# Optimization experiments

Measured on AMD Instinct MI355X. Metric: run time of the kernel, lower is better.

## Reference

```python
import jax, jax.numpy as jnp
import numpy as np

C_S, C_Z, N_HEADS = 768, 64, 12
HEAD_DIM = C_S // N_HEADS
L = 1024
EPS = 1e-5


def _ln(x, g, b):
    mu = jnp.mean(x, axis=-1, keepdims=True)
    var = jnp.mean((x - mu) ** 2, axis=-1, keepdims=True)
    return (x - mu) * jax.lax.rsqrt(var + EPS) * g + b


def setup_inputs() -> dict:
    key = jax.random.key(0)
    ks = jax.random.split(key, 12)
    w = lambda k, shp, fan_in: jax.random.normal(k, shp, dtype=jnp.float32) / np.sqrt(fan_in)
    return {
        "single": jax.random.normal(ks[0], (L, C_S), dtype=jnp.float32),
        "pair": jax.random.normal(ks[1], (L, L, C_Z), dtype=jnp.float32),
        "ln_s_g": jnp.ones((C_S,), jnp.float32),
        "ln_s_b": jnp.zeros((C_S,), jnp.float32),
        "ln_z_g": jnp.ones((C_Z,), jnp.float32),
        "ln_z_b": jnp.zeros((C_Z,), jnp.float32),
        "Wq": w(ks[2], (C_S, C_S), C_S),
        "Wk": w(ks[3], (C_S, C_S), C_S),
        "Wv": w(ks[4], (C_S, C_S), C_S),
        "Wb": w(ks[5], (C_Z, N_HEADS), C_Z),
        "Wout": w(ks[6], (C_S, C_S), C_S),
        "bout": jnp.zeros((C_S,), jnp.float32),
        "Wgate": w(ks[7], (C_S, C_S), C_S),
        "bgate": jnp.zeros((C_S,), jnp.float32),
    }


def reference(single, pair, ln_s_g, ln_s_b, ln_z_g, ln_z_b,
              Wq, Wk, Wv, Wb, Wout, bout, Wgate, bgate):
    Lq = single.shape[0]
    s = _ln(single, ln_s_g, ln_s_b)                    # [L, C_S]
    z = _ln(pair, ln_z_g, ln_z_b)                      # [L, L, C_Z]
    q = (s @ Wq).reshape(Lq, N_HEADS, HEAD_DIM)
    k = (s @ Wk).reshape(Lq, N_HEADS, HEAD_DIM)
    v = (s @ Wv).reshape(Lq, N_HEADS, HEAD_DIM)
    logits = jnp.einsum('ihd,jhd->hij', q, k) / np.sqrt(HEAD_DIM)
    logits = logits + jnp.einsum('ijc,ch->hij', z, Wb)  # pair bias per head
    attn = jax.nn.softmax(logits, axis=-1)              # [H, L, L]
    out = jnp.einsum('hij,jhd->ihd', attn, v).reshape(Lq, C_S)
    return single + jax.nn.sigmoid(s @ Wgate + bgate) * (out @ Wout + bout)
```

## Files before the change

### kernel.cpp

```cpp
#include <hip/hip_runtime.h>

#define LQ 1024
#define CS 768
#define CZ 64
#define NH 12
#define HD 64

typedef float4 f4;
using bf16x8 = __attribute__((ext_vector_type(8))) short;
using f32x4  = __attribute__((ext_vector_type(4))) float;

static __device__ __forceinline__ unsigned short f2bf(float f) {
  unsigned int u = __float_as_uint(f);
  u += 0x7fffu + ((u >> 16) & 1u);
  return (unsigned short)(u >> 16);
}
static __device__ __forceinline__ float bf2f(unsigned short b) {
  return __uint_as_float(((unsigned int)b) << 16);
}
static __device__ __forceinline__ unsigned cvtpk(float lo, float hi) {
  unsigned r;
  asm("v_cvt_pk_bf16_f32 %0, %1, %2" : "=v"(r) : "v"(lo), "v"(hi));
  return r;
}

__global__ __launch_bounds__(256) void ln_wconv_k(
    const float* __restrict__ x, const float* __restrict__ g,
    const float* __restrict__ b, unsigned short* __restrict__ s_out,
    const float* __restrict__ Wq, const float* __restrict__ Wk,
    const float* __restrict__ Wv, const float* __restrict__ Wg,
    const float* __restrict__ Wo, unsigned short* __restrict__ wt) {
  const int bid = blockIdx.x;
  const int t = threadIdx.x;
  if (bid < LQ) {
    const int row = bid;
    const float* xr = x + (size_t)row * CS;
    float v0 = xr[t], v1 = xr[t + 256], v2 = xr[t + 512];
    float s1 = v0 + v1 + v2;
    float s2 = v0 * v0 + v1 * v1 + v2 * v2;
#pragma unroll
    for (int m = 1; m < 64; m <<= 1) {
      s1 += __shfl_xor(s1, m);
      s2 += __shfl_xor(s2, m);
    }
    __shared__ float r1[4], r2[4];
    const int wid = t >> 6;
    if ((t & 63) == 0) { r1[wid] = s1; r2[wid] = s2; }
    __syncthreads();
    s1 = r1[0] + r1[1] + r1[2] + r1[3];
    s2 = r2[0] + r2[1] + r2[2] + r2[3];
    const float mu = s1 * (1.f / CS);
    const float var = s2 * (1.f / CS) - mu * mu;
    const float rs = rsqrtf(var + 1e-5f);
    s_out[(size_t)row * CS + t]       = f2bf((v0 - mu) * rs * g[t]       + b[t]);
    s_out[(size_t)row * CS + t + 256] = f2bf((v1 - mu) * rs * g[t + 256] + b[t + 256]);
    s_out[(size_t)row * CS + t + 512] = f2bf((v2 - mu) * rs * g[t + 512] + b[t + 512]);
  } else {
    int r = bid - LQ;
    const int bz = r / 144; r %= 144;
    const int n0 = (r % 12) * 64, k0 = (r / 12) * 64;
    const float* W;
    switch (bz) {
      case 0: W = Wq; break;
      case 1: W = Wk; break;
      case 2: W = Wv; break;
      case 3: W = Wg; break;
      default: W = Wo; break;
    }
    unsigned short* o = wt + (size_t)bz * CS * CS;
    __shared__ float T[64][68];
    {
      const int rr = t >> 4, c = (t & 15) * 4;
#pragma unroll
      for (int u = 0; u < 4; ++u) {
        const f4 v = *(const f4*)&W[(size_t)(k0 + rr + u * 16) * CS + n0 + c];
        *(f4*)&T[rr + u * 16][c] = v;
      }
    }
    __syncthreads();
    {
      const int rn = t >> 2, ck = (t & 3) * 16;
      __align__(16) unsigned short tmp[16];
#pragma unroll
      for (int u = 0; u < 16; ++u) tmp[u] = f2bf(T[ck + u][rn]);
      unsigned short* dst = &o[(size_t)(n0 + rn) * CS + k0 + ck];
      *(uint4*)dst = ((const uint4*)tmp)[0];
      *(uint4*)(dst + 8) = ((const uint4*)tmp)[1];
    }
  }
}

__global__ __launch_bounds__(256) void pair_k(
    const float* __restrict__ pair, const float* __restrict__ zg,
    const float* __restrict__ zb, const float* __restrict__ Wb,
    unsigned short* __restrict__ biasF) {
  const int bid = blockIdx.x;
  const int t = threadIdx.x;
  const int w = t >> 6, lane = t & 63, g = lane >> 4, c = lane & 15;
  const int i0 = (bid >> 3) * 4;
  const int j0 = (bid & 7) * 128;
  const int il = c & 3, jl = c >> 2;
  const int irow = i0 + il;
  const int g2 = g * 2;
  const int gi = i0 >> 4, ga = (i0 >> 2) & 3;
  const size_t hd_base = ((size_t)gi * 16) * 4 * 256 + (size_t)ga * 64;

  const int csafe = (c < NH) ? c : 0;
  float C1 = 0.f, C2 = 0.f;
  for (int ch = 0; ch < CZ; ++ch) {
    const float wv = (c < NH) ? Wb[ch * NH + csafe] : 0.f;
    C1 = fmaf(zg[ch], wv, C1);
    C2 = fmaf(zb[ch], wv, C2);
  }
  bf16x8 wf0, wf1;
#pragma unroll
  for (int u = 0; u < 8; ++u) {
    const float w0 = (c < NH) ? zg[g * 8 + u] * Wb[(g * 8 + u) * NH + csafe] : 0.f;
    const float w1 = (c < NH) ? zg[32 + g * 8 + u] * Wb[(32 + g * 8 + u) * NH + csafe] : 0.f;
    wf0[u] = (short)f2bf(w0);
    wf1[u] = (short)f2bf(w1);
  }

  f32x4 p00, p01, p02, p03;
  f32x4 p10, p11, p12, p13;
  {
    const f32x4* s0 = (const f32x4*)(pair + ((size_t)irow * LQ + (j0 + w * 32 + jl)) * CZ);
    p00 = s0[g2]; p01 = s0[g2 + 1]; p02 = s0[g2 + 8]; p03 = s0[g2 + 9];
  }
#pragma unroll
  for (int it = 0; it < 8; ++it) {
    const bool useA = (it & 1) == 0;
    if (it < 7) {
      const f32x4* sn = (const f32x4*)(pair + ((size_t)irow * LQ + (j0 + w * 32 + (it + 1) * 4 + jl)) * CZ);
      if (useA) { p10 = sn[g2]; p11 = sn[g2 + 1]; p12 = sn[g2 + 8]; p13 = sn[g2 + 9]; }
      else      { p00 = sn[g2]; p01 = sn[g2 + 1]; p02 = sn[g2 + 8]; p03 = sn[g2 + 9]; }
    }
    const f32x4 x0a = useA ? p00 : p10;
    const f32x4 x0b = useA ? p01 : p11;
    const f32x4 x1a = useA ? p02 : p12;
    const f32x4 x1b = useA ? p03 : p13;

    float s1 = (((x0a[0] + x0a[1]) + (x0a[2] + x0a[3])) + ((x0b[0] + x0b[1]) + (x0b[2] + x0b[3])))
             + (((x1a[0] + x1a[1]) + (x1a[2] + x1a[3])) + ((x1b[0] + x1b[1]) + (x1b[2] + x1b[3])));
    float s2 = (((x0a[0]*x0a[0] + x0a[1]*x0a[1]) + (x0a[2]*x0a[2] + x0a[3]*x0a[3]))
             +  ((x0b[0]*x0b[0] + x0b[1]*x0b[1]) + (x0b[2]*x0b[2] + x0b[3]*x0b[3])))
             + (((x1a[0]*x1a[0] + x1a[1]*x1a[1]) + (x1a[2]*x1a[2] + x1a[3]*x1a[3]))
             +  ((x1b[0]*x1b[0] + x1b[1]*x1b[1]) + (x1b[2]*x1b[2] + x1b[3]*x1b[3])));
    s1 += __shfl_xor(s1, 16); s1 += __shfl_xor(s1, 32);
    s2 += __shfl_xor(s2, 16); s2 += __shfl_xor(s2, 32);
    const float mu = s1 * (1.f / CZ);
    const float var = s2 * (1.f / CZ) - mu * mu;
    const float rs = rsqrtf(var + 1e-5f);
    const float mup = -rs * mu;

    union { unsigned u[4]; bf16x8 v8; } A, B;
    A.u[0] = cvtpk(x0a[0], x0a[1]); A.u[1] = cvtpk(x0a[2], x0a[3]);
    A.u[2] = cvtpk(x0b[0], x0b[1]); A.u[3] = cvtpk(x0b[2], x0b[3]);
    B.u[0] = cvtpk(x1a[0], x1a[1]); B.u[1] = cvtpk(x1a[2], x1a[3]);
    B.u[2] = cvtpk(x1b[0], x1b[1]); B.u[3] = cvtpk(x1b[2], x1b[3]);

    f32x4 dd = (f32x4){0.f, 0.f, 0.f, 0.f};
    dd = __builtin_amdgcn_mfma_f32_16x16x32_bf16(A.v8, wf0, dd, 0, 0, 0);
    dd = __builtin_amdgcn_mfma_f32_16x16x32_bf16(B.v8, wf1, dd, 0, 0, 0);

    const float rr0 = __shfl(rs, g * 4 + 0), mm0 = __shfl(mup, g * 4 + 0);
    const float rr1 = __shfl(rs, g * 4 + 1), mm1 = __shfl(mup, g * 4 + 1);
    const float rr2 = __shfl(rs, g * 4 + 2), mm2 = __shfl(mup, g * 4 + 2);
    const float rr3 = __shfl(rs, g * 4 + 3), mm3 = __shfl(mup, g * 4 + 3);

    if (c < NH) {
      const float b0 = fmaf(rr0, dd[0], fmaf(mm0, C1, C2));
      const float b1 = fmaf(rr1, dd[1], fmaf(mm1, C1, C2));
      const float b2 = fmaf(rr2, dd[2], fmaf(mm2, C1, C2));
      const float b3 = fmaf(rr3, dd[3], fmaf(mm3, C1, C2));
      const int jj = j0 + w * 32 + it * 4 + g;
      const size_t base = ((size_t)c * 64) * 16384
                        + hd_base
                        + (size_t)(jj >> 6) * 1024
                        + (size_t)((jj >> 4) & 3) * 256
                        + (jj & 15) * 4;
      uint2 st;
      st.x = cvtpk(b0, b1);
      st.y = cvtpk(b2, b3);
      *(uint2*)&biasF[base] = st;
    }
  }
}

__global__ __launch_bounds__(256) void gemm_qkvg_k(
    const unsigned short* __restrict__ s, const unsigned short* __restrict__ wt,
    const float* __restrict__ bg,
    unsigned short* __restrict__ qb, unsigned short* __restrict__ kb,
    unsigned short* __restrict__ vt, float* __restrict__ gpre) {
  __shared__ __align__(16) unsigned short As[64][88];
  __shared__ __align__(16) unsigned short Bs[128][88];
  const int t = threadIdx.x;
  const int w = t >> 6, lane = t & 63, g = lane >> 4, c = lane & 15;
  const int wm = w >> 1, wn = w & 1;
  const int bx = blockIdx.x % 24, by = blockIdx.x / 24;
  const int m0 = by * 64;
  const int wid = bx / 6;
  const int nl0 = (bx % 6) * 128;
  const unsigned short* B = wt + (size_t)wid * CS * CS;

  f32x4 acc[2][4];
#pragma unroll
  for (int i = 0; i < 2; ++i)
#pragma unroll
    for (int j = 0; j < 4; ++j) acc[i][j] = (f32x4){0.f, 0.f, 0.f, 0.f};

  const int sra = t >> 2, sha = (t & 3) * 16;
  const int srb = t >> 1, shb = (t & 1) * 32;
  for (int kt = 0; kt < CS; kt += 64) {
    __syncthreads();
#pragma unroll
    for (int u = 0; u < 2; ++u)
      *(uint4*)&As[sra][sha + u * 8] = *(const uint4*)&s[(size_t)(m0 + sra) * CS + kt + sha + u * 8];
#pragma unroll
    for (int u = 0; u < 4; ++u)
      *(uint4*)&Bs[srb][shb + u * 8] = *(const uint4*)&B[(size_t)(nl0 + srb) * CS + kt + shb + u * 8];
    __syncthreads();
#pragma unroll
    for (int kk = 0; kk < 64; kk += 32) {
      bf16x8 af[2], bfr[4];
#pragma unroll
      for (int i = 0; i < 2; ++i) af[i] = *(const bf16x8*)&As[wm * 32 + i * 16 + c][kk + g * 8];
#pragma unroll
      for (int j = 0; j < 4; ++j) bfr[j] = *(const bf16x8*)&Bs[wn * 64 + j * 16 + c][kk + g * 8];
#pragma unroll
      for (int i = 0; i < 2; ++i)
#pragma unroll
        for (int j = 0; j < 4; ++j)
          acc[i][j] = __builtin_amdgcn_mfma_f32_16x16x32_bf16(af[i], bfr[j], acc[i][j], 0, 0, 0);
    }
  }
#pragma unroll
  for (int i = 0; i < 2; ++i) {
#pragma unroll
    for (int j = 0; j < 4; ++j) {
      const int mb = m0 + wm * 32 + i * 16 + g * 4;
      const int nn = nl0 + wn * 64 + j * 16 + c;
      const f32x4 a = acc[i][j];
      if (wid == 0) {
#pragma unroll
        for (int r = 0; r < 4; ++r) qb[(size_t)(mb + r) * CS + nn] = f2bf(a[r] * 0.125f);
      } else if (wid == 1) {
#pragma unroll
        for (int r = 0; r < 4; ++r) kb[(size_t)(mb + r) * CS + nn] = f2bf(a[r]);
      } else if (wid == 2) {
        ushort4 pk;
        pk.x = f2bf(a[0]); pk.y = f2bf(a[1]); pk.z = f2bf(a[2]); pk.w = f2bf(a[3]);
        *(ushort4*)&vt[(size_t)nn * LQ + mb] = pk;
      } else {
        const float bb = bg[nn];
#pragma unroll
        for (int r = 0; r < 4; ++r) gpre[(size_t)(mb + r) * CS + nn] = a[r] + bb;
      }
    }
  }
}

__global__ __launch_bounds__(256) void attn_k(
    const unsigned short* __restrict__ q, const unsigned short* __restrict__ k,
    const unsigned short* __restrict__ vt, const unsigned short* __restrict__ biasF,
    float* __restrict__ Opart, float* __restrict__ ml) {
  __shared__ __align__(16) unsigned short Qs[64][88];
  __shared__ __align__(16) unsigned short Ks[2][64][88];
  __shared__ __align__(16) unsigned short Vts[2][64][88];
  __shared__ __align__(16) unsigned short Ps[4][16][88];
  const int bx = blockIdx.x, h = blockIdx.y, z = blockIdx.z;
  const int i0 = bx * 64;
  const int jb = z * 512;
  const int t = threadIdx.x;
  const int w = t >> 6, lane = t & 63, g = lane >> 4, c = lane & 15;
  const int sr = t >> 2, sc = (t & 3) * 16;

#pragma unroll
  for (int u = 0; u < 2; ++u) {
    *(uint4*)&Qs[sr][sc + u * 8]     = *(const uint4*)&q[(size_t)(i0 + sr) * CS + h * HD + sc + u * 8];
    *(uint4*)&Ks[0][sr][sc + u * 8]  = *(const uint4*)&k[(size_t)(jb + sr) * CS + h * HD + sc + u * 8];
    *(uint4*)&Vts[0][sr][sc + u * 8] = *(const uint4*)&vt[(size_t)(h * HD + sr) * LQ + jb + sc + u * 8];
  }
  const size_t bbase = ((((size_t)h * 64 + (bx * 4 + w)) * 16 + (size_t)z * 8) * 4) * 256 + lane * 4;
  ushort4 bcur[4];
#pragma unroll
  for (int nb = 0; nb < 4; ++nb) bcur[nb] = *(const ushort4*)&biasF[bbase + nb * 256];
  __syncthreads();

  const bf16x8 aq0 = *(const bf16x8*)&Qs[w * 16 + c][g * 8];
  const bf16x8 aq1 = *(const bf16x8*)&Qs[w * 16 + c][32 + g * 8];

  f32x4 acc_o[4];
#pragma unroll
  for (int nb = 0; nb < 4; ++nb) acc_o[nb] = (f32x4){0.f, 0.f, 0.f, 0.f};
  float m_run[4] = {-1e30f, -1e30f, -1e30f, -1e30f};
  float l_run[4] = {0.f, 0.f, 0.f, 0.f};

  for (int jt = 0; jt < 8; ++jt) {
    const int cur = jt & 1;
    uint4 kr0, kr1, vr0, vr1;
    ushort4 bnx[4];
    if (jt < 7) {
      const int jn = jb + (jt + 1) * 64;
      kr0 = *(const uint4*)&k[(size_t)(jn + sr) * CS + h * HD + sc];
      kr1 = *(const uint4*)&k[(size_t)(jn + sr) * CS + h * HD + sc + 8];
      vr0 = *(const uint4*)&vt[(size_t)(h * HD + sr) * LQ + jn + sc];
      vr1 = *(const uint4*)&vt[(size_t)(h * HD + sr) * LQ + jn + sc + 8];
#pragma unroll
      for (int nb = 0; nb < 4; ++nb)
        bnx[nb] = *(const ushort4*)&biasF[bbase + (size_t)(jt + 1) * 1024 + nb * 256];
    }

    f32x4 sa[4];
#pragma unroll
    for (int nb = 0; nb < 4; ++nb) {
      f32x4 ci;
      ci[0] = bf2f(bcur[nb].x); ci[1] = bf2f(bcur[nb].y);
      ci[2] = bf2f(bcur[nb].z); ci[3] = bf2f(bcur[nb].w);
      const bf16x8 b0 = *(const bf16x8*)&Ks[cur][nb * 16 + c][g * 8];
      const bf16x8 b1 = *(const bf16x8*)&Ks[cur][nb * 16 + c][32 + g * 8];
      ci = __builtin_amdgcn_mfma_f32_16x16x32_bf16(aq0, b0, ci, 0, 0, 0);
      ci = __builtin_amdgcn_mfma_f32_16x16x32_bf16(aq1, b1, ci, 0, 0, 0);
      sa[nb] = ci;
    }

    float mt[4];
#pragma unroll
    for (int r = 0; r < 4; ++r) {
      float v = fmaxf(fmaxf(sa[0][r], sa[1][r]), fmaxf(sa[2][r], sa[3][r]));
      v = fmaxf(v, __shfl_xor(v, 1));
      v = fmaxf(v, __shfl_xor(v, 2));
      v = fmaxf(v, __shfl_xor(v, 4));
      v = fmaxf(v, __shfl_xor(v, 8));
      mt[r] = v;
    }
    float scale[4], ps[4];
#pragma unroll
    for (int r = 0; r < 4; ++r) {
      const float mn = fmaxf(m_run[r], mt[r]);
      scale[r] = __expf(m_run[r] - mn);
      m_run[r] = mn;
      ps[r] = 0.f;
    }
#pragma unroll
    for (int nb = 0; nb < 4; ++nb) {
#pragma unroll
      for (int r = 0; r < 4; ++r) {
        const float p = __expf(sa[nb][r] - m_run[r]);
        ps[r] += p;
        Ps[w][g * 4 + r][nb * 16 + c] = f2bf(p);
      }
    }
#pragma unroll
    for (int r = 0; r < 4; ++r) {
      float v = ps[r];
      v += __shfl_xor(v, 1);
      v += __shfl_xor(v, 2);
      v += __shfl_xor(v, 4);
      v += __shfl_xor(v, 8);
      l_run[r] = l_run[r] * scale[r] + v;
#pragma unroll
      for (int nb = 0; nb < 4; ++nb) acc_o[nb][r] *= scale[r];
    }

#pragma unroll
    for (int kb = 0; kb < 2; ++kb) {
      const bf16x8 pa = *(const bf16x8*)&Ps[w][c][kb * 32 + g * 8];
#pragma unroll
      for (int nb = 0; nb < 4; ++nb) {
        const bf16x8 bv = *(const bf16x8*)&Vts[cur][nb * 16 + c][kb * 32 + g * 8];
        acc_o[nb] = __builtin_amdgcn_mfma_f32_16x16x32_bf16(pa, bv, acc_o[nb], 0, 0, 0);
      }
    }

    if (jt < 7) {
      *(uint4*)&Ks[cur ^ 1][sr][sc]      = kr0;
      *(uint4*)&Ks[cur ^ 1][sr][sc + 8]  = kr1;
      *(uint4*)&Vts[cur ^ 1][sr][sc]     = vr0;
      *(uint4*)&Vts[cur ^ 1][sr][sc + 8] = vr1;
      __syncthreads();
#pragma unroll
      for (int nb = 0; nb < 4; ++nb) bcur[nb] = bnx[nb];
    }
  }

  const size_t rowb = (size_t)(z * NH + h) * LQ + i0 + w * 16 + g * 4;
#pragma unroll
  for (int nb = 0; nb < 4; ++nb)
#pragma unroll
    for (int r = 0; r < 4; ++r)
      Opart[(rowb + r) * HD + nb * 16 + c] = acc_o[nb][r];
  if (c == 0) {
#pragma unroll
    for (int r = 0; r < 4; ++r) {
      ml[(rowb + r) * 2]     = m_run[r];
      ml[(rowb + r) * 2 + 1] = l_run[r];
    }
  }
}

__global__ __launch_bounds__(256) void combine_k(
    const float* __restrict__ Opart, const float* __restrict__ ml,
    unsigned short* __restrict__ attno) {
  const int t = threadIdx.x;
  const int row = blockIdx.x * 4 + (t >> 6);
  const int d = t & 63;
  const int h = row >> 10, i = row & 1023;
  const size_t r0 = (size_t)h * LQ + i;
  const size_t r1 = (size_t)(NH + h) * LQ + i;
  const float m0 = ml[r0 * 2], l0 = ml[r0 * 2 + 1];
  const float m1 = ml[r1 * 2], l1 = ml[r1 * 2 + 1];
  const float M = fmaxf(m0, m1);
  const float a0 = __expf(m0 - M), a1 = __expf(m1 - M);
  const float L = a0 * l0 + a1 * l1;
  const float o = (a0 * Opart[r0 * HD + d] + a1 * Opart[r1 * HD + d]) / L;
  attno[(size_t)i * CS + h * HD + d] = f2bf(o);
}

__global__ __launch_bounds__(256) void gemm_final_k(
    const unsigned short* __restrict__ A, const unsigned short* __restrict__ wt,
    const float* __restrict__ bout, const float* __restrict__ single,
    const float* __restrict__ gpre, float* __restrict__ out) {
  __shared__ __align__(16) unsigned short As[64][88];
  __shared__ __align__(16) unsigned short Bs[128][88];
  const int t = threadIdx.x;
  const int wave = t >> 6, lane = t & 63, g = lane >> 4, c = lane & 15;
  const int wm = wave >> 1, wn = wave & 1;
  const int m0 = blockIdx.y * 64;
  const int nl0 = blockIdx.x * 128;
  const unsigned short* B = wt + (size_t)4 * CS * CS;

  f32x4 acc[2][4];
#pragma unroll
  for (int i = 0; i < 2; ++i)
#pragma unroll
    for (int j = 0; j < 4; ++j) acc[i][j] = (f32x4){0.f, 0.f, 0.f, 0.f};

  const int sra = t >> 2, sha = (t & 3) * 16;
  const int srb = t >> 1, shb = (t & 1) * 32;
  for (int kt = 0; kt < CS; kt += 64) {
    __syncthreads();
#pragma unroll
    for (int u = 0; u < 2; ++u)
      *(uint4*)&As[sra][sha + u * 8] = *(const uint4*)&A[(size_t)(m0 + sra) * CS + kt + sha + u * 8];
#pragma unroll
    for (int u = 0; u < 4; ++u)
      *(uint4*)&Bs[srb][shb + u * 8] = *(const uint4*)&B[(size_t)(nl0 + srb) * CS + kt + shb + u * 8];
    __syncthreads();
#pragma unroll
    for (int kk = 0; kk < 64; kk += 32) {
      bf16x8 af[2], bfr[4];
#pragma unroll
      for (int i = 0; i < 2; ++i) af[i] = *(const bf16x8*)&As[wm * 32 + i * 16 + c][kk + g * 8];
#pragma unroll
      for (int j = 0; j < 4; ++j) bfr[j] = *(const bf16x8*)&Bs[wn * 64 + j * 16 + c][kk + g * 8];
#pragma unroll
      for (int i = 0; i < 2; ++i)
#pragma unroll
        for (int j = 0; j < 4; ++j)
          acc[i][j] = __builtin_amdgcn_mfma_f32_16x16x32_bf16(af[i], bfr[j], acc[i][j], 0, 0, 0);
    }
  }

#pragma unroll
  for (int i = 0; i < 2; ++i) {
#pragma unroll
    for (int j = 0; j < 4; ++j) {
      const int mb = m0 + wm * 32 + i * 16 + g * 4;
      const int nn = nl0 + wn * 64 + j * 16 + c;
      const float bb = bout[nn];
      const f32x4 a = acc[i][j];
#pragma unroll
      for (int r = 0; r < 4; ++r) {
        const size_t idx = (size_t)(mb + r) * CS + nn;
        const float gate = 1.f / (1.f + __expf(-gpre[idx]));
        out[idx] = single[idx] + gate * (a[r] + bb);
      }
    }
  }
}

extern "C" void kernel_launch(void* const* d_in, const int* in_sizes, int n_in,
                              void* d_out, int out_size, void* d_ws, size_t ws_size,
                              hipStream_t stream) {
  const float* single = (const float*)d_in[0];
  const float* pair   = (const float*)d_in[1];
  const float* ln_s_g = (const float*)d_in[2];
  const float* ln_s_b = (const float*)d_in[3];
  const float* ln_z_g = (const float*)d_in[4];
  const float* ln_z_b = (const float*)d_in[5];
  const float* Wq     = (const float*)d_in[6];
  const float* Wk     = (const float*)d_in[7];
  const float* Wv     = (const float*)d_in[8];
  const float* Wb     = (const float*)d_in[9];
  const float* Wout   = (const float*)d_in[10];
  const float* bout   = (const float*)d_in[11];
  const float* Wgate  = (const float*)d_in[12];
  const float* bgate  = (const float*)d_in[13];
  float* out = (float*)d_out;

  unsigned short* s_bf  = (unsigned short*)d_ws;
  unsigned short* wt    = s_bf  + (size_t)LQ * CS;
  unsigned short* q_bf  = wt    + (size_t)5 * CS * CS;
  unsigned short* k_bf  = q_bf  + (size_t)LQ * CS;
  unsigned short* vt_bf = k_bf  + (size_t)LQ * CS;
  unsigned short* attno = vt_bf + (size_t)CS * LQ;
  unsigned short* biasF = attno + (size_t)LQ * CS;
  float* gpre  = (float*)(biasF + (size_t)NH * LQ * LQ);
  float* Opart = gpre  + (size_t)LQ * CS;
  float* mlw   = Opart + (size_t)2 * NH * LQ * HD;

  hipLaunchKernelGGL(pair_k, dim3(2048), dim3(256), 0, stream,
                     pair, ln_z_g, ln_z_b, Wb, biasF);
  hipLaunchKernelGGL(ln_wconv_k, dim3(LQ + 720), dim3(256), 0, stream,
                     single, ln_s_g, ln_s_b, s_bf, Wq, Wk, Wv, Wgate, Wout, wt);
  hipLaunchKernelGGL(gemm_qkvg_k, dim3(384), dim3(256), 0, stream,
                     s_bf, wt, bgate, q_bf, k_bf, vt_bf, gpre);
  hipLaunchKernelGGL(attn_k, dim3(16, NH, 2), dim3(256), 0, stream,
                     q_bf, k_bf, vt_bf, biasF, Opart, mlw);
  hipLaunchKernelGGL(combine_k, dim3(3072), dim3(256), 0, stream,
                     Opart, mlw, attno);
  hipLaunchKernelGGL(gemm_final_k, dim3(6, 16), dim3(256), 0, stream,
                     attno, wt, bout, single, gpre, out);
}
```

Measured before the change: 127.6 us.

## Stage pair tile in swizzled LDS with coalesced loads before bias MFMA

pair_k now loads each block's 4x64x64 pair tile with fully coalesced float4 reads, converts it to bf16 and stores it in XOR-swizzled shared memory. LayerNorm statistics are computed per row from LDS (computed from the bf16-rounded values) and kept in shared arrays, and the MFMA reads operands from LDS. Grid doubles to 4096 smaller blocks. The aim is better global-load coalescing and memory parallelism for the dominant pair read. In exchange it adds about 33KB of LDS per block, which limits occupancy, plus two barriers, and the statistics lose some precision.

```diff
diff --git a/kernel.cpp b/kernel.cpp
--- a/kernel.cpp
+++ b/kernel.cpp
@@ -94,16 +94,18 @@
     const float* __restrict__ pair, const float* __restrict__ zg,
     const float* __restrict__ zb, const float* __restrict__ Wb,
     unsigned short* __restrict__ biasF) {
-  const int bid = blockIdx.x;
+  __shared__ __align__(16) unsigned short zs[256 * 64];
+  __shared__ float rstats[256], mstats[256];
   const int t = threadIdx.x;
   const int w = t >> 6, lane = t & 63, g = lane >> 4, c = lane & 15;
-  const int i0 = (bid >> 3) * 4;
-  const int j0 = (bid & 7) * 128;
-  const int il = c & 3, jl = c >> 2;
-  const int irow = i0 + il;
-  const int g2 = g * 2;
-  const int gi = i0 >> 4, ga = (i0 >> 2) & 3;
-  const size_t hd_base = ((size_t)gi * 16) * 4 * 256 + (size_t)ga * 64;
+  const int bid = blockIdx.x;
+  const int i0 = (bid >> 4) * 4;
+  const int j0 = (bid & 15) * 64;
+
+  const f32x4* src = (const f32x4*)(pair + ((size_t)(i0 + w) * LQ + j0) * CZ);
+  f32x4 vv[16];
+#pragma unroll
+  for (int u = 0; u < 16; ++u) vv[u] = src[u * 64 + lane];
 
   const int csafe = (c < NH) ? c : 0;
   float C1 = 0.f, C2 = 0.f;
@@ -121,61 +123,68 @@
     wf1[u] = (short)f2bf(w1);
   }
 
-  f32x4 p00, p01, p02, p03;
-  f32x4 p10, p11, p12, p13;
+#pragma unroll
+  for (int u = 0; u < 16; ++u) {
+    const int idx = u * 64 + lane;
+    const int j = idx >> 4;
+    const int kq = idx & 15;
+    const int row = w * 64 + j;
+    const int chunk = kq >> 1, half = kq & 1;
+    uint2 pk;
+    pk.x = cvtpk(vv[u][0], vv[u][1]);
+    pk.y = cvtpk(vv[u][2], vv[u][3]);
+    *(uint2*)&zs[row * 64 + ((chunk ^ (row & 7)) << 3) + (half << 2)] = pk;
+  }
+  __syncthreads();
+
   {
-    const f32x4* s0 = (const f32x4*)(pair + ((size_t)irow * LQ + (j0 + w * 32 + jl)) * CZ);
-    p00 = s0[g2]; p01 = s0[g2 + 1]; p02 = s0[g2 + 8]; p03 = s0[g2 + 9];
-  }
-#pragma unroll
-  for (int it = 0; it < 8; ++it) {
-    const bool useA = (it & 1) == 0;
-    if (it < 7) {
-      const f32x4* sn = (const f32x4*)(pair + ((size_t)irow * LQ + (j0 + w * 32 + (it + 1) * 4 + jl)) * CZ);
-      if (useA) { p10 = sn[g2]; p11 = sn[g2 + 1]; p12 = sn[g2 + 8]; p13 = sn[g2 + 9]; }
-      else      { p00 = sn[g2]; p01 = sn[g2 + 1]; p02 = sn[g2 + 8]; p03 = sn[g2 + 9]; }
-    }
-    const f32x4 x0a = useA ? p00 : p10;
-    const f32x4 x0b = useA ? p01 : p11;
-    const f32x4 x1a = useA ? p02 : p12;
-    const f32x4 x1b = useA ? p03 : p13;
-
-    float s1 = (((x0a[0] + x0a[1]) + (x0a[2] + x0a[3])) + ((x0b[0] + x0b[1]) + (x0b[2] + x0b[3])))
-             + (((x1a[0] + x1a[1]) + (x1a[2] + x1a[3])) + ((x1b[0] + x1b[1]) + (x1b[2] + x1b[3])));
-    float s2 = (((x0a[0]*x0a[0] + x0a[1]*x0a[1]) + (x0a[2]*x0a[2] + x0a[3]*x0a[3]))
-             +  ((x0b[0]*x0b[0] + x0b[1]*x0b[1]) + (x0b[2]*x0b[2] + x0b[3]*x0b[3])))
-             + (((x1a[0]*x1a[0] + x1a[1]*x1a[1]) + (x1a[2]*x1a[2] + x1a[3]*x1a[3]))
-             +  ((x1b[0]*x1b[0] + x1b[1]*x1b[1]) + (x1b[2]*x1b[2] + x1b[3]*x1b[3])));
-    s1 += __shfl_xor(s1, 16); s1 += __shfl_xor(s1, 32);
-    s2 += __shfl_xor(s2, 16); s2 += __shfl_xor(s2, 32);
+    float s1 = 0.f, s2 = 0.f;
+    const int r7 = t & 7;
+#pragma unroll
+    for (int k = 0; k < 8; ++k) {
+      const uint4 q = *(const uint4*)&zs[t * 64 + ((k ^ r7) << 3)];
+      const float f0 = __uint_as_float(q.x << 16), f1 = __uint_as_float(q.x & 0xffff0000u);
+      const float f2 = __uint_as_float(q.y << 16), f3 = __uint_as_float(q.y & 0xffff0000u);
+      const float f4v = __uint_as_float(q.z << 16), f5 = __uint_as_float(q.z & 0xffff0000u);
+      const float f6 = __uint_as_float(q.w << 16), f7 = __uint_as_float(q.w & 0xffff0000u);
+      s1 += ((f0 + f1) + (f2 + f3)) + ((f4v + f5) + (f6 + f7));
+      s2 += ((f0 * f0 + f1 * f1) + (f2 * f2 + f3 * f3))
+          + ((f4v * f4v + f5 * f5) + (f6 * f6 + f7 * f7));
+    }
     const float mu = s1 * (1.f / CZ);
     const float var = s2 * (1.f / CZ) - mu * mu;
     const float rs = rsqrtf(var + 1e-5f);
-    const float mup = -rs * mu;
-
-    union { unsigned u[4]; bf16x8 v8; } A, B;
-    A.u[0] = cvtpk(x0a[0], x0a[1]); A.u[1] = cvtpk(x0a[2], x0a[3]);
-    A.u[2] = cvtpk(x0b[0], x0b[1]); A.u[3] = cvtpk(x0b[2], x0b[3]);
-    B.u[0] = cvtpk(x1a[0], x1a[1]); B.u[1] = cvtpk(x1a[2], x1a[3]);
-    B.u[2] = cvtpk(x1b[0], x1b[1]); B.u[3] = cvtpk(x1b[2], x1b[3]);
-
+    rstats[t] = rs;
+    mstats[t] = -rs * mu;
+  }
+  __syncthreads();
+
+  const int il = c & 3, jl = c >> 2;
+  const int gi = i0 >> 4, ga = (i0 >> 2) & 3;
+  const size_t hd_base = ((size_t)gi * 16) * 4 * 256 + (size_t)ga * 64;
+#pragma unroll
+  for (int mm = 0; mm < 4; ++mm) {
+    const int jloc = w * 16 + mm * 4;
+    const int arow = il * 64 + jloc + jl;
+    const int r7a = arow & 7;
+    const bf16x8 a0 = *(const bf16x8*)&zs[arow * 64 + ((g ^ r7a) << 3)];
+    const bf16x8 a1 = *(const bf16x8*)&zs[arow * 64 + (((4 + g) ^ r7a) << 3)];
     f32x4 dd = (f32x4){0.f, 0.f, 0.f, 0.f};
-    dd = __builtin_amdgcn_mfma_f32_16x16x32_bf16(A.v8, wf0, dd, 0, 0, 0);
-    dd = __builtin_amdgcn_mfma_f32_16x16x32_bf16(B.v8, wf1, dd, 0, 0, 0);
-
-    const float rr0 = __shfl(rs, g * 4 + 0), mm0 = __shfl(mup, g * 4 + 0);
-    const float rr1 = __shfl(rs, g * 4 + 1), mm1 = __shfl(mup, g * 4 + 1);
-    const float rr2 = __shfl(rs, g * 4 + 2), mm2 = __shfl(mup, g * 4 + 2);
-    const float rr3 = __shfl(rs, g * 4 + 3), mm3 = __shfl(mup, g * 4 + 3);
-
+    dd = __builtin_amdgcn_mfma_f32_16x16x32_bf16(a0, wf0, dd, 0, 0, 0);
+    dd = __builtin_amdgcn_mfma_f32_16x16x32_bf16(a1, wf1, dd, 0, 0, 0);
+
+    const int jg = jloc + g;
+    const float rs0 = rstats[jg],       mp0 = mstats[jg];
+    const float rs1 = rstats[64 + jg],  mp1 = mstats[64 + jg];
+    const float rs2 = rstats[128 + jg], mp2 = mstats[128 + jg];
+    const float rs3 = rstats[192 + jg], mp3 = mstats[192 + jg];
     if (c < NH) {
-      const float b0 = fmaf(rr0, dd[0], fmaf(mm0, C1, C2));
-      const float b1 = fmaf(rr1, dd[1], fmaf(mm1, C1, C2));
-      const float b2 = fmaf(rr2, dd[2], fmaf(mm2, C1, C2));
-      const float b3 = fmaf(rr3, dd[3], fmaf(mm3, C1, C2));
-      const int jj = j0 + w * 32 + it * 4 + g;
-      const size_t base = ((size_t)c * 64) * 16384
-                        + hd_base
+      const float b0 = fmaf(rs0, dd[0], fmaf(mp0, C1, C2));
+      const float b1 = fmaf(rs1, dd[1], fmaf(mp1, C1, C2));
+      const float b2 = fmaf(rs2, dd[2], fmaf(mp2, C1, C2));
+      const float b3 = fmaf(rs3, dd[3], fmaf(mp3, C1, C2));
+      const int jj = j0 + jg;
+      const size_t base = ((size_t)c * 64) * 16384 + hd_base
                         + (size_t)(jj >> 6) * 1024
                         + (size_t)((jj >> 4) & 3) * 256
                         + (jj & 15) * 4;
@@ -510,7 +519,7 @@
   float* Opart = gpre  + (size_t)LQ * CS;
   float* mlw   = Opart + (size_t)2 * NH * LQ * HD;
 
-  hipLaunchKernelGGL(pair_k, dim3(2048), dim3(256), 0, stream,
+  hipLaunchKernelGGL(pair_k, dim3(4096), dim3(256), 0, stream,
                      pair, ln_z_g, ln_z_b, Wb, biasF);
   hipLaunchKernelGGL(ln_wconv_k, dim3(LQ + 720), dim3(256), 0, stream,
                      single, ln_s_g, ln_s_b, s_bf, Wq, Wk, Wv, Wgate, Wout, wt);
```

New measurement: 130.1 us. Within noise of the previous version (+1.9%).
